# Kernel optimization log

Hardware: AMD Instinct MI355X
Metric: run time of the kernel (lower is better)

The kernel has to match this reference:

```python
import jax, jax.numpy as jnp
import numpy as np

B, S, D, H = 8, 1024, 256, 16
HD = D // H  # head_dim = 16
THETA = 10000.0


def rope(x):
    # Faithful to RotaryEmbeddings: integer-division exponent, 1-indexed
    # positions, rotor = sin + i*cos (real part is sin).
    b, s, d = x.shape
    i = jnp.arange(0, d, 2)
    expo = (2 * i) // d  # integer division: 0 for first half, 1 for second
    thetas = 1.0 / (THETA ** expo.astype(jnp.float32))  # [d/2]
    pos = jnp.arange(s, dtype=jnp.float32) + 1.0  # 1-indexed positions
    ang = pos[:, None] * thetas[None, :]  # [s, d/2]
    sin, cos = jnp.sin(ang), jnp.cos(ang)
    xp = x.reshape(b, s, d // 2, 2)
    xe, xo = xp[..., 0], xp[..., 1]  # consecutive pairs (view_as_complex)
    # (xe + i*xo) * (sin + i*cos)
    real = xe * sin - xo * cos
    imag = xe * cos + xo * sin
    return jnp.stack((real, imag), axis=-1).reshape(b, s, d)


def setup_inputs() -> dict:
    key = jax.random.key(0)
    ks = jax.random.split(key, 9)
    sc = 1.0 / np.sqrt(D)
    return {
        "x": jax.random.normal(ks[0], (B, S, D), dtype=jnp.float32),
        "wq_w": jax.random.normal(ks[1], (D, D), dtype=jnp.float32) * sc,
        "wq_b": jax.random.normal(ks[2], (D,), dtype=jnp.float32) * 0.01,
        "wk_w": jax.random.normal(ks[3], (D, D), dtype=jnp.float32) * sc,
        "wk_b": jax.random.normal(ks[4], (D,), dtype=jnp.float32) * 0.01,
        "wv_w": jax.random.normal(ks[5], (D, D), dtype=jnp.float32) * sc,
        "wv_b": jax.random.normal(ks[6], (D,), dtype=jnp.float32) * 0.01,
        "wo_w": jax.random.normal(ks[7], (D, D), dtype=jnp.float32) * sc,
        "wo_b": jax.random.normal(ks[8], (D,), dtype=jnp.float32) * 0.01,
    }


def reference(x, wq_w, wq_b, wk_w, wk_b, wv_w, wv_b, wo_w, wo_b):
    b, s, d = x.shape
    q = x @ wq_w.T + wq_b
    k = x @ wk_w.T + wk_b  # computed in original but dead in no-cache path
    v = x @ wv_w.T + wv_b
    del k
    xq = rope(q).reshape(b, s, H, HD).transpose(0, 2, 1, 3)  # [b,h,s,hd]
    xv = rope(v).reshape(b, s, H, HD).transpose(0, 2, 1, 3)  # [b,h,s,hd]
    # no-cache path: keys = xq (rotated queries), values = rotated v; NO softmax
    scores = jnp.einsum('bhqd,bhkd->bhqk', xq, xq) / jnp.sqrt(jnp.float32(HD))
    att = jnp.einsum('bhqk,bhkd->bhqd', scores, xv)  # [b,h,s,hd]
    att = att.transpose(0, 2, 1, 3).reshape(b, s, d)
    return att @ wo_w.T + wo_b
```

## Files before the change

### kernel.cpp

```cpp
#include <hip/hip_runtime.h>

#define Gz 8192
#define Dz 256
#define Sz 1024

typedef _Float16 half8 __attribute__((ext_vector_type(8)));
typedef float    floatx4 __attribute__((ext_vector_type(4)));

#define GLOAD_LDS(gptr, lptr)                                                      \
    __builtin_amdgcn_global_load_lds(                                              \
        (const __attribute__((address_space(1))) void*)(gptr),                     \
        (__attribute__((address_space(3))) void*)(lptr), 16, 0, 0)

__device__ inline half8 cvt8(const float* __restrict__ p) {
    float4 a = ((const float4*)p)[0];
    float4 b = ((const float4*)p)[1];
    half8 h;
    h[0]=(_Float16)a.x; h[1]=(_Float16)a.y; h[2]=(_Float16)a.z; h[3]=(_Float16)a.w;
    h[4]=(_Float16)b.x; h[5]=(_Float16)b.y; h[6]=(_Float16)b.z; h[7]=(_Float16)b.w;
    return h;
}

__global__ __launch_bounds__(256) void convert_kernel(
    const float* __restrict__ x, const float* __restrict__ wq,
    const float* __restrict__ wv,
    _Float16* __restrict__ x16, _Float16* __restrict__ w16)
{
    size_t e = ((size_t)blockIdx.x * 256 + threadIdx.x) * 8;
    const float* src;
    _Float16* dst;
    if (e < (size_t)Gz * Dz) { src = x + e; dst = x16 + e; }
    else {
        size_t e2 = e - (size_t)Gz * Dz;
        dst = w16 + e2;
        src = (e2 < 65536) ? (wq + e2) : (wv + (e2 - 65536));
    }
    *(half8*)dst = cvt8(src);
}

__global__ __launch_bounds__(256) void qv_gemm_rope(
    const _Float16* __restrict__ x16, const _Float16* __restrict__ w16,
    const float* __restrict__ bq, const float* __restrict__ bv,
    _Float16* __restrict__ xq, _Float16* __restrict__ xv)
{
    __shared__ _Float16 As[128 * 64];
    __shared__ _Float16 Bs[128 * 64];
    const int t = threadIdx.x, lane = t & 63, w = t >> 6;
    const int g0 = blockIdx.x * 128;
    const int by = blockIdx.y;
    const int n0 = by * 128;
    const int wm = (w >> 1) * 64, wn = (w & 1) * 64;
    const int fr = lane & 15, kq = lane >> 4;

    floatx4 acc[4][4] = {};

    for (int k0 = 0; k0 < Dz; k0 += 64) {
        __syncthreads();
        #pragma unroll
        for (int p = 0; p < 4; ++p) {
            const int flat = (t + 256 * p) * 8;
            const int row = flat >> 6, col = flat & 63;
            GLOAD_LDS(x16 + (size_t)(g0 + row) * Dz + k0 + col, &As[flat]);
            GLOAD_LDS(w16 + (size_t)(n0 + row) * Dz + k0 + col, &Bs[flat]);
        }
        __syncthreads();
        #pragma unroll
        for (int ks = 0; ks < 2; ++ks) {
            const int kk = ks * 32 + kq * 8;
            half8 a[4], b[4];
            #pragma unroll
            for (int i = 0; i < 4; ++i) a[i] = *(const half8*)&As[(wm + i * 16 + fr) * 64 + kk];
            #pragma unroll
            for (int j = 0; j < 4; ++j) b[j] = *(const half8*)&Bs[(wn + j * 16 + fr) * 64 + kk];
            #pragma unroll
            for (int i = 0; i < 4; ++i)
                #pragma unroll
                for (int j = 0; j < 4; ++j)
                    acc[i][j] = __builtin_amdgcn_mfma_f32_16x16x32_f16(a[i], b[j], acc[i][j], 0, 0, 0);
        }
    }

    const int qside = (by < 2);
    const float* bias = qside ? bq : bv;
    _Float16* outp = qside ? xq : xv;
    const float theta = (by & 1) ? 1e-4f : 1.0f;
    const float sign  = (fr & 1) ? 1.0f : -1.0f;

    float sn[4][4], cs[4][4];
    #pragma unroll
    for (int i = 0; i < 4; ++i)
        #pragma unroll
        for (int r = 0; r < 4; ++r) {
            const int g = g0 + wm + i * 16 + kq * 4 + r;
            const float pos = (float)((g & (Sz - 1)) + 1);
            __sincosf(pos * theta, &sn[i][r], &cs[i][r]);
        }

    #pragma unroll
    for (int j = 0; j < 4; ++j) {
        const int ch = (by & 1) * 128 + wn + j * 16 + fr;
        const float bcol = bias[ch];
        #pragma unroll
        for (int i = 0; i < 4; ++i)
            #pragma unroll
            for (int r = 0; r < 4; ++r) {
                const int g = g0 + wm + i * 16 + kq * 4 + r;
                float v = acc[i][j][r] + bcol;
                float other = __shfl_xor(v, 1, 64);
                outp[(size_t)g * Dz + ch] =
                    (_Float16)(v * sn[i][r] + sign * other * cs[i][r]);
            }
    }
}

__global__ __launch_bounds__(256) void head_outer(
    const _Float16* __restrict__ xq, const _Float16* __restrict__ xv,
    float* __restrict__ Mpart)
{
    __shared__ __align__(16) _Float16 qsT[16][136];
    __shared__ __align__(16) _Float16 vsT[16][136];
    const int t = threadIdx.x;
    const int bh = blockIdx.x;
    const int b = bh >> 4, h = bh & 15;
    const size_t base = (size_t)b * Sz * Dz + (size_t)blockIdx.y * 128 * Dz + h * 16;

    {
        const int s = t >> 1, eg = t & 1;
        half8 q8 = *(const half8*)&xq[base + (size_t)s * Dz + eg * 8];
        half8 v8 = *(const half8*)&xv[base + (size_t)s * Dz + eg * 8];
        #pragma unroll
        for (int i = 0; i < 8; ++i) {
            qsT[eg * 8 + i][s] = q8[i];
            vsT[eg * 8 + i][s] = v8[i];
        }
    }
    __syncthreads();

    const int e = t >> 4, f = t & 15;
    float acc = 0.f;
    #pragma unroll
    for (int s0 = 0; s0 < 128; s0 += 8) {
        half8 q8 = *(const half8*)&qsT[e][s0];
        half8 v8 = *(const half8*)&vsT[f][s0];
        #pragma unroll
        for (int i = 0; i < 8; ++i) acc += (float)q8[i] * (float)v8[i];
    }
    Mpart[((size_t)blockIdx.y * 128 + bh) * 256 + t] = acc;
}

__global__ __launch_bounds__(256) void make_p(
    const float* __restrict__ Mpart, const float* __restrict__ Wo,
    _Float16* __restrict__ Pt)
{
    __shared__ float Ms[256];
    const int t = threadIdx.x;
    const int bh = blockIdx.x;
    const int b = bh >> 4, h = bh & 15;
    float s = 0.f;
    #pragma unroll
    for (int c = 0; c < 8; ++c) s += Mpart[((size_t)c * 128 + bh) * 256 + t];
    Ms[t] = s * 0.25f;
    __syncthreads();

    const int c = t;
    float wo[16];
    const float4* wop = (const float4*)&Wo[(size_t)c * Dz + h * 16];
    #pragma unroll
    for (int q = 0; q < 4; ++q) {
        float4 v = wop[q];
        wo[4*q+0] = v.x; wo[4*q+1] = v.y; wo[4*q+2] = v.z; wo[4*q+3] = v.w;
    }
    half8 lo, hi;
    #pragma unroll
    for (int e = 0; e < 16; ++e) {
        float a = 0.f;
        #pragma unroll
        for (int f = 0; f < 16; ++f) a = fmaf(Ms[e * 16 + f], wo[f], a);
        if (e < 8) lo[e] = (_Float16)a; else hi[e - 8] = (_Float16)a;
    }
    _Float16* dst = &Pt[((size_t)(b * 256 + c)) * Dz + h * 16];
    *(half8*)dst       = lo;
    *(half8*)(dst + 8) = hi;
}

__global__ __launch_bounds__(256) void out_gemm(
    const _Float16* __restrict__ xq, const _Float16* __restrict__ Pt,
    const float* __restrict__ bo, float* __restrict__ out)
{
    __shared__ _Float16 As[64 * 64];
    __shared__ _Float16 Bs[128 * 64];
    const int t = threadIdx.x, lane = t & 63, w = t >> 6;
    const int g0 = blockIdx.x * 64;
    const int n0 = blockIdx.y * 128;
    const int b  = g0 >> 10;
    const int wm = (w >> 1) * 32, wn = (w & 1) * 64;
    const int fr = lane & 15, kq = lane >> 4;
    const _Float16* Pb = Pt + (size_t)b * 256 * Dz;

    floatx4 acc[2][4] = {};

    for (int k0 = 0; k0 < Dz; k0 += 64) {
        __syncthreads();
        #pragma unroll
        for (int p = 0; p < 2; ++p) {
            const int flat = (t + 256 * p) * 8;
            const int row = flat >> 6, col = flat & 63;
            GLOAD_LDS(xq + (size_t)(g0 + row) * Dz + k0 + col, &As[flat]);
        }
        #pragma unroll
        for (int p = 0; p < 4; ++p) {
            const int flat = (t + 256 * p) * 8;
            const int row = flat >> 6, col = flat & 63;
            GLOAD_LDS(Pb + (size_t)(n0 + row) * Dz + k0 + col, &Bs[flat]);
        }
        __syncthreads();
        #pragma unroll
        for (int ks = 0; ks < 2; ++ks) {
            const int kk = ks * 32 + kq * 8;
            half8 a[2], bf[4];
            #pragma unroll
            for (int i = 0; i < 2; ++i) a[i] = *(const half8*)&As[(wm + i * 16 + fr) * 64 + kk];
            #pragma unroll
            for (int j = 0; j < 4; ++j) bf[j] = *(const half8*)&Bs[(wn + j * 16 + fr) * 64 + kk];
            #pragma unroll
            for (int i = 0; i < 2; ++i)
                #pragma unroll
                for (int j = 0; j < 4; ++j)
                    acc[i][j] = __builtin_amdgcn_mfma_f32_16x16x32_f16(a[i], bf[j], acc[i][j], 0, 0, 0);
        }
    }

    #pragma unroll
    for (int j = 0; j < 4; ++j) {
        const int c = n0 + wn + j * 16 + fr;
        const float bcol = bo[c];
        #pragma unroll
        for (int i = 0; i < 2; ++i)
            #pragma unroll
            for (int r = 0; r < 4; ++r) {
                const int g = g0 + wm + i * 16 + kq * 4 + r;
                out[(size_t)g * Dz + c] = acc[i][j][r] + bcol;
            }
    }
}

extern "C" void kernel_launch(void* const* d_in, const int* in_sizes, int n_in,
                              void* d_out, int out_size, void* d_ws, size_t ws_size,
                              hipStream_t stream)
{
    const float* x    = (const float*)d_in[0];
    const float* wq_w = (const float*)d_in[1];
    const float* wq_b = (const float*)d_in[2];
    const float* wv_w = (const float*)d_in[5];
    const float* wv_b = (const float*)d_in[6];
    const float* wo_w = (const float*)d_in[7];
    const float* wo_b = (const float*)d_in[8];

    _Float16* x16  = (_Float16*)d_ws;
    _Float16* w16  = x16  + (size_t)Gz * Dz;
    _Float16* xq16 = w16  + 131072;
    _Float16* xv16 = xq16 + (size_t)Gz * Dz;
    _Float16* Pt   = xv16 + (size_t)Gz * Dz;
    float*    Mpart = (float*)(Pt + 524288);
    float*    out  = (float*)d_out;

    convert_kernel<<<dim3((Gz * Dz + 131072) / 2048), 256, 0, stream>>>(
        x, wq_w, wv_w, x16, w16);
    qv_gemm_rope<<<dim3(Gz / 128, 4), 256, 0, stream>>>(
        x16, w16, wq_b, wv_b, xq16, xv16);
    head_outer<<<dim3(128, 8), 256, 0, stream>>>(xq16, xv16, Mpart);
    make_p<<<dim3(128), 256, 0, stream>>>(Mpart, wo_w, Pt);
    out_gemm<<<dim3(Gz / 64, 2), 256, 0, stream>>>(xq16, Pt, wo_b, out);
}
```

Measured before the change: 104.4 us.

## Fuse fp16 conversion into QV GEMM and merge head outer-product with P construction

Removes the separate fp32-to-fp16 convert kernel. The QV GEMM now loads fp32 x and weights directly, converts them in registers, and stores them to an XOR-swizzled LDS layout to avoid bank conflicts. It also merges the head_outer and make_p kernels into a single 512-thread kernel per batch-head that loops over the whole sequence, using fdot2 and an in-block reduction. This cuts two launches and the x16 and Mpart round trips through global memory. The cost is only 128 blocks for the head reduction (less parallelism) and no async global-to-LDS loads in the GEMM.

```diff
diff --git a/kernel.cpp b/kernel.cpp
--- a/kernel.cpp
+++ b/kernel.cpp
@@ -4,7 +4,9 @@
 #define Dz 256
 #define Sz 1024
 
-typedef _Float16 half8 __attribute__((ext_vector_type(8)));
+typedef _Float16 half8  __attribute__((ext_vector_type(8)));
+typedef _Float16 half4  __attribute__((ext_vector_type(4)));
+typedef _Float16 half2v __attribute__((ext_vector_type(2)));
 typedef float    floatx4 __attribute__((ext_vector_type(4)));
 
 #define GLOAD_LDS(gptr, lptr)                                                      \
@@ -12,66 +14,65 @@
         (const __attribute__((address_space(1))) void*)(gptr),                     \
         (__attribute__((address_space(3))) void*)(lptr), 16, 0, 0)
 
-__device__ inline half8 cvt8(const float* __restrict__ p) {
-    float4 a = ((const float4*)p)[0];
-    float4 b = ((const float4*)p)[1];
-    half8 h;
+__device__ inline half4 cvt4(float4 a) {
+    half4 h;
     h[0]=(_Float16)a.x; h[1]=(_Float16)a.y; h[2]=(_Float16)a.z; h[3]=(_Float16)a.w;
-    h[4]=(_Float16)b.x; h[5]=(_Float16)b.y; h[6]=(_Float16)b.z; h[7]=(_Float16)b.w;
     return h;
 }
 
-__global__ __launch_bounds__(256) void convert_kernel(
+__global__ __launch_bounds__(256) void qv_gemm_rope(
     const float* __restrict__ x, const float* __restrict__ wq,
     const float* __restrict__ wv,
-    _Float16* __restrict__ x16, _Float16* __restrict__ w16)
-{
-    size_t e = ((size_t)blockIdx.x * 256 + threadIdx.x) * 8;
-    const float* src;
-    _Float16* dst;
-    if (e < (size_t)Gz * Dz) { src = x + e; dst = x16 + e; }
-    else {
-        size_t e2 = e - (size_t)Gz * Dz;
-        dst = w16 + e2;
-        src = (e2 < 65536) ? (wq + e2) : (wv + (e2 - 65536));
-    }
-    *(half8*)dst = cvt8(src);
-}
-
-__global__ __launch_bounds__(256) void qv_gemm_rope(
-    const _Float16* __restrict__ x16, const _Float16* __restrict__ w16,
     const float* __restrict__ bq, const float* __restrict__ bv,
     _Float16* __restrict__ xq, _Float16* __restrict__ xv)
 {
-    __shared__ _Float16 As[128 * 64];
-    __shared__ _Float16 Bs[128 * 64];
+    __shared__ __align__(16) _Float16 As[128 * 64];
+    __shared__ __align__(16) _Float16 Bs[128 * 64];
     const int t = threadIdx.x, lane = t & 63, w = t >> 6;
     const int g0 = blockIdx.x * 128;
     const int by = blockIdx.y;
-    const int n0 = by * 128;
     const int wm = (w >> 1) * 64, wn = (w & 1) * 64;
     const int fr = lane & 15, kq = lane >> 4;
+    const float* wsrc = ((by < 2) ? wq : wv) + (size_t)(by & 1) * 128 * Dz;
+
+    char* Ab = (char*)As;
+    char* Bb = (char*)Bs;
 
     floatx4 acc[4][4] = {};
 
     for (int k0 = 0; k0 < Dz; k0 += 64) {
-        __syncthreads();
-        #pragma unroll
-        for (int p = 0; p < 4; ++p) {
-            const int flat = (t + 256 * p) * 8;
-            const int row = flat >> 6, col = flat & 63;
-            GLOAD_LDS(x16 + (size_t)(g0 + row) * Dz + k0 + col, &As[flat]);
-            GLOAD_LDS(w16 + (size_t)(n0 + row) * Dz + k0 + col, &Bs[flat]);
+        float4 a4[8], b4[8];
+        #pragma unroll
+        for (int p = 0; p < 8; ++p) {
+            const int id = t + 256 * p;
+            const int row = id >> 4, c4 = id & 15;
+            a4[p] = *(const float4*)(x    + (size_t)(g0 + row) * Dz + k0 + c4 * 4);
+            b4[p] = *(const float4*)(wsrc + (size_t)row        * Dz + k0 + c4 * 4);
+        }
+        __syncthreads();
+        #pragma unroll
+        for (int p = 0; p < 8; ++p) {
+            const int id = t + 256 * p;
+            const int row = id >> 4, cb = (id & 15) * 8;
+            const int off = row * 128 + (cb ^ ((row & 7) << 4));
+            *(half4*)(Ab + off) = cvt4(a4[p]);
+            *(half4*)(Bb + off) = cvt4(b4[p]);
         }
         __syncthreads();
         #pragma unroll
         for (int ks = 0; ks < 2; ++ks) {
-            const int kk = ks * 32 + kq * 8;
+            const int kb = (ks * 32 + kq * 8) * 2;
             half8 a[4], b[4];
             #pragma unroll
-            for (int i = 0; i < 4; ++i) a[i] = *(const half8*)&As[(wm + i * 16 + fr) * 64 + kk];
-            #pragma unroll
-            for (int j = 0; j < 4; ++j) b[j] = *(const half8*)&Bs[(wn + j * 16 + fr) * 64 + kk];
+            for (int i = 0; i < 4; ++i) {
+                const int r = wm + i * 16 + fr;
+                a[i] = *(const half8*)(Ab + r * 128 + (kb ^ ((r & 7) << 4)));
+            }
+            #pragma unroll
+            for (int j = 0; j < 4; ++j) {
+                const int r = wn + j * 16 + fr;
+                b[j] = *(const half8*)(Bb + r * 128 + (kb ^ ((r & 7) << 4)));
+            }
             #pragma unroll
             for (int i = 0; i < 4; ++i)
                 #pragma unroll
@@ -113,74 +114,76 @@
     }
 }
 
-__global__ __launch_bounds__(256) void head_outer(
+__global__ __launch_bounds__(512) void head_p(
     const _Float16* __restrict__ xq, const _Float16* __restrict__ xv,
-    float* __restrict__ Mpart)
-{
-    __shared__ __align__(16) _Float16 qsT[16][136];
-    __shared__ __align__(16) _Float16 vsT[16][136];
+    const float* __restrict__ wo, _Float16* __restrict__ Pt)
+{
+    __shared__ __align__(16) _Float16 qsT[16][264];
+    __shared__ __align__(16) _Float16 vsT[16][264];
+    __shared__ float red[512];
+    __shared__ float Ms[256];
+
     const int t = threadIdx.x;
     const int bh = blockIdx.x;
     const int b = bh >> 4, h = bh & 15;
-    const size_t base = (size_t)b * Sz * Dz + (size_t)blockIdx.y * 128 * Dz + h * 16;
-
-    {
-        const int s = t >> 1, eg = t & 1;
-        half8 q8 = *(const half8*)&xq[base + (size_t)s * Dz + eg * 8];
-        half8 v8 = *(const half8*)&xv[base + (size_t)s * Dz + eg * 8];
+    const size_t base = (size_t)b * Sz * Dz + h * 16;
+
+    const int s  = t >> 1, eg = t & 1;
+    const int e  = (t >> 4) & 15, f = t & 15;
+    const int hf = t >> 8;
+
+    float acc = 0.f;
+    for (int it = 0; it < 4; ++it) {
+        const size_t roff = base + (size_t)(it * 256 + s) * Dz + eg * 8;
+        half8 q8 = *(const half8*)&xq[roff];
+        half8 v8 = *(const half8*)&xv[roff];
+        __syncthreads();
         #pragma unroll
         for (int i = 0; i < 8; ++i) {
             qsT[eg * 8 + i][s] = q8[i];
             vsT[eg * 8 + i][s] = v8[i];
         }
-    }
+        __syncthreads();
+        #pragma unroll
+        for (int s0 = 0; s0 < 128; s0 += 8) {
+            half8 q = *(const half8*)&qsT[e][hf * 128 + s0];
+            half8 v = *(const half8*)&vsT[f][hf * 128 + s0];
+#if __has_builtin(__builtin_amdgcn_fdot2)
+            #pragma unroll
+            for (int k = 0; k < 4; ++k) {
+                half2v a2 = {q[2*k], q[2*k+1]};
+                half2v b2 = {v[2*k], v[2*k+1]};
+                acc = __builtin_amdgcn_fdot2(a2, b2, acc, false);
+            }
+#else
+            #pragma unroll
+            for (int k = 0; k < 8; ++k) acc += (float)q[k] * (float)v[k];
+#endif
+        }
+    }
+    red[t] = acc;
     __syncthreads();
-
-    const int e = t >> 4, f = t & 15;
-    float acc = 0.f;
-    #pragma unroll
-    for (int s0 = 0; s0 < 128; s0 += 8) {
-        half8 q8 = *(const half8*)&qsT[e][s0];
-        half8 v8 = *(const half8*)&vsT[f][s0];
-        #pragma unroll
-        for (int i = 0; i < 8; ++i) acc += (float)q8[i] * (float)v8[i];
-    }
-    Mpart[((size_t)blockIdx.y * 128 + bh) * 256 + t] = acc;
-}
-
-__global__ __launch_bounds__(256) void make_p(
-    const float* __restrict__ Mpart, const float* __restrict__ Wo,
-    _Float16* __restrict__ Pt)
-{
-    __shared__ float Ms[256];
-    const int t = threadIdx.x;
-    const int bh = blockIdx.x;
-    const int b = bh >> 4, h = bh & 15;
-    float s = 0.f;
-    #pragma unroll
-    for (int c = 0; c < 8; ++c) s += Mpart[((size_t)c * 128 + bh) * 256 + t];
-    Ms[t] = s * 0.25f;
+    if (t < 256) Ms[t] = (red[t] + red[t + 256]) * 0.25f;
     __syncthreads();
 
-    const int c = t;
-    float wo[16];
-    const float4* wop = (const float4*)&Wo[(size_t)c * Dz + h * 16];
-    #pragma unroll
-    for (int q = 0; q < 4; ++q) {
-        float4 v = wop[q];
-        wo[4*q+0] = v.x; wo[4*q+1] = v.y; wo[4*q+2] = v.z; wo[4*q+3] = v.w;
-    }
-    half8 lo, hi;
-    #pragma unroll
-    for (int e = 0; e < 16; ++e) {
+    const int c = t >> 1;
+    float wv_[16];
+    const float4* wop = (const float4*)&wo[(size_t)c * Dz + h * 16];
+    #pragma unroll
+    for (int q4 = 0; q4 < 4; ++q4) {
+        float4 v4 = wop[q4];
+        wv_[4*q4+0] = v4.x; wv_[4*q4+1] = v4.y; wv_[4*q4+2] = v4.z; wv_[4*q4+3] = v4.w;
+    }
+    half8 r;
+    #pragma unroll
+    for (int ee = 0; ee < 8; ++ee) {
+        const int e_ = eg * 8 + ee;
         float a = 0.f;
         #pragma unroll
-        for (int f = 0; f < 16; ++f) a = fmaf(Ms[e * 16 + f], wo[f], a);
-        if (e < 8) lo[e] = (_Float16)a; else hi[e - 8] = (_Float16)a;
-    }
-    _Float16* dst = &Pt[((size_t)(b * 256 + c)) * Dz + h * 16];
-    *(half8*)dst       = lo;
-    *(half8*)(dst + 8) = hi;
+        for (int ff = 0; ff < 16; ++ff) a = fmaf(Ms[e_ * 16 + ff], wv_[ff], a);
+        r[ee] = (_Float16)a;
+    }
+    *(half8*)&Pt[((size_t)(b * 256 + c)) * Dz + h * 16 + eg * 8] = r;
 }
 
 __global__ __launch_bounds__(256) void out_gemm(
@@ -256,19 +259,13 @@
     const float* wo_w = (const float*)d_in[7];
     const float* wo_b = (const float*)d_in[8];
 
-    _Float16* x16  = (_Float16*)d_ws;
-    _Float16* w16  = x16  + (size_t)Gz * Dz;
-    _Float16* xq16 = w16  + 131072;
+    _Float16* xq16 = (_Float16*)d_ws;
     _Float16* xv16 = xq16 + (size_t)Gz * Dz;
     _Float16* Pt   = xv16 + (size_t)Gz * Dz;
-    float*    Mpart = (float*)(Pt + 524288);
     float*    out  = (float*)d_out;
 
-    convert_kernel<<<dim3((Gz * Dz + 131072) / 2048), 256, 0, stream>>>(
-        x, wq_w, wv_w, x16, w16);
     qv_gemm_rope<<<dim3(Gz / 128, 4), 256, 0, stream>>>(
-        x16, w16, wq_b, wv_b, xq16, xv16);
-    head_outer<<<dim3(128, 8), 256, 0, stream>>>(xq16, xv16, Mpart);
-    make_p<<<dim3(128), 256, 0, stream>>>(Mpart, wo_w, Pt);
+        x, wq_w, wv_w, wq_b, wv_b, xq16, xv16);
+    head_p<<<dim3(128), 512, 0, stream>>>(xq16, xv16, wo_w, Pt);
     out_gemm<<<dim3(Gz / 64, 2), 256, 0, stream>>>(xq16, Pt, wo_b, out);
 }
```

New measurement: 100.7 us. 3.5% less time.
